# Kernel tuning notes

Measured on AMD Instinct MI355X. Metric: run time of the kernel, lower is better.

## Reference

```python
import jax, jax.numpy as jnp
import numpy as np

NUM_HEADS = 16
D_MODEL = 1024
BATCH = 4
SEQ = 1024


def setup_inputs() -> dict:
    key = jax.random.key(0)
    k_x, k_m, k_wqkv, k_bqkv, k_wo, k_bo = jax.random.split(key, 6)
    d = D_MODEL
    scale = 1.0 / np.sqrt(d)
    return {
        "x": jax.random.normal(k_x, (BATCH, SEQ, d), dtype=jnp.float32),
        "mask": jax.random.randint(k_m, (BATCH, SEQ, SEQ), 0, 2, dtype=jnp.int32),
        "Wqkv": jax.random.normal(k_wqkv, (d, 3 * d), dtype=jnp.float32) * scale,
        "bqkv": jax.random.normal(k_bqkv, (3 * d,), dtype=jnp.float32) * 0.02,
        "Wo": jax.random.normal(k_wo, (d, d), dtype=jnp.float32) * scale,
        "bo": jax.random.normal(k_bo, (d,), dtype=jnp.float32) * 0.02,
    }


def reference(x, mask, Wqkv, bqkv, Wo, bo):
    B, S, D = x.shape
    H = NUM_HEADS
    hd = D // H
    # fused QKV projection: [B,S,3D] -> [B,S,H,3*hd] -> [B,H,S,3*hd]
    qkv = (x @ Wqkv + bqkv).reshape(B, S, H, 3 * hd).transpose(0, 2, 1, 3)
    q, k, v = jnp.split(qkv, 3, axis=-1)  # each [B,H,S,hd]
    # scores [B,H,S,S], scaled by sqrt(head_dim)
    scores = jnp.einsum("bhqd,bhkd->bhqk", q, k) / jnp.sqrt(jnp.float32(hd))
    scores = jnp.where(mask[:, None, :, :] == 0, jnp.float32(-1e20), scores)
    attn = jax.nn.softmax(scores, axis=-1)
    vals = jnp.einsum("bhqk,bhkd->bhqd", attn, v)  # [B,H,S,hd]
    vals = vals.transpose(0, 2, 1, 3).reshape(B, S, D)
    return vals @ Wo + bo
```

## Files before the change

kernel.cpp:

```cpp
#include <hip/hip_runtime.h>
#include <cstddef>
#include <cstdint>

#define BATCH 4
#define SEQ   1024
#define DM    1024
#define NH    16
#define HD    64
#define D3    3072
#define LOG2E 1.44269504088896340736f
#define QSCALE (0.125f * LOG2E)

typedef _Float16 f16x8 __attribute__((ext_vector_type(8)));
typedef _Float16 f16x4 __attribute__((ext_vector_type(4)));
typedef __fp16   h16x2 __attribute__((ext_vector_type(2)));
typedef float    f32x4 __attribute__((ext_vector_type(4)));

#define MFMA16(a, b, c) __builtin_amdgcn_mfma_f32_16x16x32_f16((a), (b), (c), 0, 0, 0)
#define GLD_LDS16(gp, lp) \
  __builtin_amdgcn_global_load_lds((const __attribute__((address_space(1))) unsigned int*)(gp), \
                                   (__attribute__((address_space(3))) unsigned int*)(lp), 16, 0, 0)
#if __has_builtin(__builtin_amdgcn_exp2f)
#define EXP2(x) __builtin_amdgcn_exp2f(x)
#else
#define EXP2(x) exp2f(x)
#endif

__global__ __launch_bounds__(256) void prep(const float* __restrict__ x,
                                            _Float16* __restrict__ x16,
                                            const int* __restrict__ mask,
                                            unsigned long long* __restrict__ mb) {
  const int tid = threadIdx.x;
  if (blockIdx.x < 2048) {
    const int i = blockIdx.x * 256 + tid;
    float4 a = ((const float4*)x)[i * 2];
    float4 b = ((const float4*)x)[i * 2 + 1];
    f16x8 o;
    o[0] = (_Float16)a.x; o[1] = (_Float16)a.y; o[2] = (_Float16)a.z; o[3] = (_Float16)a.w;
    o[4] = (_Float16)b.x; o[5] = (_Float16)b.y; o[6] = (_Float16)b.z; o[7] = (_Float16)b.w;
    ((f16x8*)x16)[i] = o;
  } else {
    const size_t i = (size_t)(blockIdx.x - 2048) * 256 + tid;
    const int m = mask[i];
    unsigned long long bits = __ballot(m != 0);
    if ((tid & 63) == 0) mb[i >> 6] = bits;
  }
}

__global__ __launch_bounds__(256) void transpose_cast2(const float* __restrict__ W1,
                                                       _Float16* __restrict__ WT1,
                                                       const float* __restrict__ W2,
                                                       _Float16* __restrict__ WT2) {
  __shared__ _Float16 T[64 * 72];
  const int tid = threadIdx.x;
  const bool first = blockIdx.x < 48;
  const float* W = first ? W1 : W2;
  _Float16* WT = first ? WT1 : WT2;
  const int N = first ? D3 : DM;
  const int K = DM;
  const int c0 = (first ? blockIdx.x : (blockIdx.x - 48)) * 64;
  const int r0 = blockIdx.y * 64;
#pragma unroll
  for (int it = 0; it < 4; ++it) {
    const int row = it * 16 + (tid >> 4);
    const int col4 = (tid & 15) * 4;
    float4 wv = *(const float4*)(W + (size_t)(r0 + row) * N + c0 + col4);
    T[(col4 + 0) * 72 + row] = (_Float16)wv.x;
    T[(col4 + 1) * 72 + row] = (_Float16)wv.y;
    T[(col4 + 2) * 72 + row] = (_Float16)wv.z;
    T[(col4 + 3) * 72 + row] = (_Float16)wv.w;
  }
  __syncthreads();
#pragma unroll
  for (int it = 0; it < 2; ++it) {
    const int g = it * 256 + tid;
    const int col = g >> 3, seg = g & 7;
    *(f16x8*)(WT + (size_t)(c0 + col) * K + r0 + seg * 8) = *(const f16x8*)(T + col * 72 + seg * 8);
  }
}

template <typename OutT, bool QKV, int TN>
__global__ __launch_bounds__(256) void gemm_bt(const _Float16* __restrict__ A,
                                               const _Float16* __restrict__ BT,
                                               const float* __restrict__ bias,
                                               OutT* __restrict__ C,
                                               _Float16* __restrict__ vTp,
                                               int M, int N, int K) {
  constexpr int NT = TN / 32;
  __shared__ _Float16 As[128 * 64];
  __shared__ _Float16 Bs[TN * 64];
  const int tid = threadIdx.x;
  const int l15 = tid & 15;
  const int quad = (tid & 63) >> 4;
  const int w = tid >> 6;
  const int wm = w >> 1, wn = w & 1;
  const int rowbase = blockIdx.y * 128;
  const int colbase = blockIdx.x * TN;

  f32x4 acc[4][NT];
#pragma unroll
  for (int mt = 0; mt < 4; ++mt)
#pragma unroll
    for (int nt = 0; nt < NT; ++nt) acc[mt][nt] = (f32x4){0.f, 0.f, 0.f, 0.f};

  for (int k0 = 0; k0 < K; k0 += 64) {
    __syncthreads();
#pragma unroll
    for (int it = 0; it < 4; ++it) {
      const int g = it * 256 + tid;
      const int r = g >> 3, cs = (g & 7) ^ (r & 7);
      GLD_LDS16(A + (size_t)(rowbase + r) * K + k0 + cs * 8, As + g * 8);
    }
#pragma unroll
    for (int it = 0; it < TN / 32; ++it) {
      const int g = it * 256 + tid;
      const int r = g >> 3, cs = (g & 7) ^ (r & 7);
      GLD_LDS16(BT + (size_t)(colbase + r) * K + k0 + cs * 8, Bs + g * 8);
    }
    __syncthreads();
#pragma unroll
    for (int kh = 0; kh < 2; ++kh) {
      f16x8 a[4], b[NT];
#pragma unroll
      for (int mt = 0; mt < 4; ++mt) {
        const int row = wm * 64 + mt * 16 + l15;
        a[mt] = *(const f16x8*)(As + row * 64 + (((kh * 4 + quad) ^ (row & 7)) << 3));
      }
#pragma unroll
      for (int nt = 0; nt < NT; ++nt) {
        const int row = wn * (TN / 2) + nt * 16 + l15;
        b[nt] = *(const f16x8*)(Bs + row * 64 + (((kh * 4 + quad) ^ (row & 7)) << 3));
      }
#pragma unroll
      for (int mt = 0; mt < 4; ++mt)
#pragma unroll
        for (int nt = 0; nt < NT; ++nt)
          acc[mt][nt] = MFMA16(a[mt], b[nt], acc[mt][nt]);
    }
  }

  float bv[NT];
#pragma unroll
  for (int nt = 0; nt < NT; ++nt) bv[nt] = bias[colbase + wn * (TN / 2) + nt * 16 + l15];
#pragma unroll
  for (int mt = 0; mt < 4; ++mt)
#pragma unroll
    for (int nt = 0; nt < NT; ++nt) {
      const int col = colbase + wn * (TN / 2) + nt * 16 + l15;
      if (QKV) {
        const int reg3 = (col >> 6) % 3;
        if (reg3 == 2) {
          const int hh = col / 192;
          const int d = col - hh * 192 - 128;
          const int row0 = rowbase + wm * 64 + mt * 16 + quad * 4;
          const int bb = row0 >> 10, s0 = row0 & 1023;
          f16x4 pk;
#pragma unroll
          for (int r = 0; r < 4; ++r) pk[r] = (_Float16)(acc[mt][nt][r] + bv[nt]);
          *(f16x4*)(vTp + ((size_t)((bb * NH + hh) * HD + d)) * SEQ + s0) = pk;
        } else {
          const float sc = (reg3 == 0) ? QSCALE : 1.f;
#pragma unroll
          for (int r = 0; r < 4; ++r) {
            const int row = rowbase + wm * 64 + mt * 16 + quad * 4 + r;
            C[(size_t)row * N + col] = (OutT)((acc[mt][nt][r] + bv[nt]) * sc);
          }
        }
      } else {
#pragma unroll
        for (int r = 0; r < 4; ++r) {
          const int row = rowbase + wm * 64 + mt * 16 + quad * 4 + r;
          C[(size_t)row * N + col] = (OutT)(acc[mt][nt][r] + bv[nt]);
        }
      }
    }
}

__global__ __launch_bounds__(256) void attn(const _Float16* __restrict__ qkv,
                                            const _Float16* __restrict__ vT,
                                            const unsigned long long* __restrict__ mb,
                                            _Float16* __restrict__ vals) {
  __shared__ _Float16 Ks[64 * 72];
  __shared__ _Float16 Vt[64 * 72];
  __shared__ _Float16 Ps[4][32 * 72];
  __shared__ __align__(8) _Float16 LUT[16][4];
  const int tid = threadIdx.x;
  const int l15 = tid & 15, quad = (tid & 63) >> 4, w = tid >> 6;
  const int i = blockIdx.x;
  const int bh = (i >> 6) * 8 + (i & 7);
  const int b = bh >> 4, h = bh & 15;
  const int q0 = ((i >> 3) & 7) << 7;

  if (tid < 16) {
    LUT[tid][0] = (tid & 1) ? (_Float16)1.f : (_Float16)0.f;
    LUT[tid][1] = (tid & 2) ? (_Float16)1.f : (_Float16)0.f;
    LUT[tid][2] = (tid & 4) ? (_Float16)1.f : (_Float16)0.f;
    LUT[tid][3] = (tid & 8) ? (_Float16)1.f : (_Float16)0.f;
  }

  const _Float16* qb = qkv + (size_t)b * SEQ * D3 + h * 192;
  f16x8 qf[2][2];
#pragma unroll
  for (int qn = 0; qn < 2; ++qn)
#pragma unroll
    for (int hf = 0; hf < 2; ++hf)
      qf[qn][hf] = *(const f16x8*)(qb + (size_t)(q0 + w * 32 + qn * 16 + l15) * D3 +
                                   hf * 32 + quad * 8);

  const _Float16* kg = qb + 64;
  const _Float16* vg = vT + (size_t)((b * NH + h) * HD) * SEQ;
  const int sr = tid >> 3, sseg = tid & 7;
  const int vd = tid >> 2, vs = tid & 3;
  const size_t mb0 = (size_t)(b * SEQ + q0 + w * 32 + l15) * 16;
  const size_t mb1 = (size_t)(b * SEQ + q0 + w * 32 + 16 + l15) * 16;

  f16x8 k0r = *(const f16x8*)(kg + (size_t)sr * D3 + sseg * 8);
  f16x8 k1r = *(const f16x8*)(kg + (size_t)(sr + 32) * D3 + sseg * 8);
  f16x8 v0r = *(const f16x8*)(vg + (size_t)vd * SEQ + vs * 8);
  f16x8 v1r = *(const f16x8*)(vg + (size_t)vd * SEQ + 32 + vs * 8);
  unsigned long long mr0 = mb[mb0], mr1 = mb[mb1];

  f32x4 lacc[2];
  f32x4 o_[2][4];
#pragma unroll
  for (int qn = 0; qn < 2; ++qn) {
    lacc[qn] = (f32x4){0.f, 0.f, 0.f, 0.f};
#pragma unroll
    for (int dt = 0; dt < 4; ++dt) o_[qn][dt] = (f32x4){0.f, 0.f, 0.f, 0.f};
  }
  f16x8 ones;
#pragma unroll
  for (int i2 = 0; i2 < 8; ++i2) ones[i2] = (_Float16)1.f;

  for (int kt = 0; kt < 16; ++kt) {
    if (kt) __syncthreads();
    *(f16x8*)(Ks + sr * 72 + sseg * 8) = k0r;
    *(f16x8*)(Ks + (sr + 32) * 72 + sseg * 8) = k1r;
    *(f16x8*)(Vt + vd * 72 + vs * 8) = v0r;
    *(f16x8*)(Vt + vd * 72 + 32 + vs * 8) = v1r;
    __syncthreads();
    const unsigned long long mc[2] = {mr0, mr1};
    if (kt < 15) {
      const int kn = (kt + 1) << 6;
      k0r = *(const f16x8*)(kg + (size_t)(kn + sr) * D3 + sseg * 8);
      k1r = *(const f16x8*)(kg + (size_t)(kn + sr + 32) * D3 + sseg * 8);
      v0r = *(const f16x8*)(vg + (size_t)vd * SEQ + kn + vs * 8);
      v1r = *(const f16x8*)(vg + (size_t)vd * SEQ + kn + 32 + vs * 8);
      mr0 = mb[mb0 + kt + 1];
      mr1 = mb[mb1 + kt + 1];
    }
    f32x4 st[4][2];
#pragma unroll
    for (int mt = 0; mt < 4; ++mt)
#pragma unroll
      for (int qn = 0; qn < 2; ++qn) st[mt][qn] = (f32x4){0.f, 0.f, 0.f, 0.f};
#pragma unroll
    for (int mt = 0; mt < 4; ++mt) {
      f16x8 ka0 = *(const f16x8*)(Ks + (mt * 16 + l15) * 72 + quad * 8);
      f16x8 ka1 = *(const f16x8*)(Ks + (mt * 16 + l15) * 72 + 32 + quad * 8);
#pragma unroll
      for (int qn = 0; qn < 2; ++qn) {
        st[mt][qn] = MFMA16(ka0, qf[qn][0], st[mt][qn]);
        st[mt][qn] = MFMA16(ka1, qf[qn][1], st[mt][qn]);
      }
    }
#pragma unroll
    for (int qn = 0; qn < 2; ++qn)
#pragma unroll
      for (int mt = 0; mt < 4; ++mt) {
        float e0 = EXP2(fminf(st[mt][qn][0], 15.f));
        float e1 = EXP2(fminf(st[mt][qn][1], 15.f));
        float e2 = EXP2(fminf(st[mt][qn][2], 15.f));
        float e3 = EXP2(fminf(st[mt][qn][3], 15.f));
        h16x2 lo = __builtin_amdgcn_cvt_pkrtz(e0, e1);
        h16x2 hi = __builtin_amdgcn_cvt_pkrtz(e2, e3);
        f16x4 pk;
        pk[0] = (_Float16)lo[0]; pk[1] = (_Float16)lo[1];
        pk[2] = (_Float16)hi[0]; pk[3] = (_Float16)hi[1];
        const unsigned nib = (unsigned)(mc[qn] >> (mt * 16 + quad * 4)) & 15u;
        pk *= *(const f16x4*)LUT[nib];
        *(f16x4*)(&Ps[w][(qn * 16 + l15) * 72 + mt * 16 + quad * 4]) = pk;
      }
    f16x8 pa[2][2];
#pragma unroll
    for (int qn = 0; qn < 2; ++qn) {
      pa[qn][0] = *(const f16x8*)(&Ps[w][(qn * 16 + l15) * 72 + quad * 8]);
      pa[qn][1] = *(const f16x8*)(&Ps[w][(qn * 16 + l15) * 72 + 32 + quad * 8]);
      lacc[qn] = MFMA16(pa[qn][0], ones, lacc[qn]);
      lacc[qn] = MFMA16(pa[qn][1], ones, lacc[qn]);
    }
#pragma unroll
    for (int dt = 0; dt < 4; ++dt) {
      f16x8 vb0 = *(const f16x8*)(Vt + (dt * 16 + l15) * 72 + quad * 8);
      f16x8 vb1 = *(const f16x8*)(Vt + (dt * 16 + l15) * 72 + 32 + quad * 8);
#pragma unroll
      for (int qn = 0; qn < 2; ++qn) {
        o_[qn][dt] = MFMA16(pa[qn][0], vb0, o_[qn][dt]);
        o_[qn][dt] = MFMA16(pa[qn][1], vb1, o_[qn][dt]);
      }
    }
  }
#pragma unroll
  for (int qn = 0; qn < 2; ++qn) {
    f32x4 inv;
#pragma unroll
    for (int r = 0; r < 4; ++r) inv[r] = 1.f / lacc[qn][r];
#pragma unroll
    for (int dt = 0; dt < 4; ++dt)
#pragma unroll
      for (int r = 0; r < 4; ++r)
        vals[(size_t)(b * SEQ + q0 + w * 32 + qn * 16 + quad * 4 + r) * DM +
             h * HD + dt * 16 + l15] = (_Float16)(o_[qn][dt][r] * inv[r]);
  }
}

extern "C" void kernel_launch(void* const* d_in, const int* in_sizes, int n_in,
                              void* d_out, int out_size, void* d_ws, size_t ws_size,
                              hipStream_t stream) {
  const float* x    = (const float*)d_in[0];
  const int*   mask = (const int*)  d_in[1];
  const float* Wqkv = (const float*)d_in[2];
  const float* bqkv = (const float*)d_in[3];
  const float* Wo   = (const float*)d_in[4];
  const float* bo   = (const float*)d_in[5];
  float* out = (float*)d_out;

  char* ws = (char*)d_ws;
  _Float16* qkv16  = (_Float16*)ws;                    ws += (size_t)BATCH*SEQ*D3*2;
  _Float16* vT16   = (_Float16*)ws;                    ws += (size_t)BATCH*DM*SEQ*2;
  _Float16* x16    = (_Float16*)ws;                    ws += (size_t)BATCH*SEQ*DM*2;
  _Float16* WqkvT  = (_Float16*)ws;                    ws += (size_t)DM*D3*2;
  _Float16* WoT    = (_Float16*)ws;                    ws += (size_t)DM*DM*2;
  _Float16* vals16 = (_Float16*)ws;                    ws += (size_t)BATCH*SEQ*DM*2;
  unsigned long long* mbits = (unsigned long long*)ws;

  prep<<<2048 + (BATCH*SEQ*SEQ)/256, 256, 0, stream>>>(x, x16, mask, mbits);
  transpose_cast2<<<dim3(64, 16), 256, 0, stream>>>(Wqkv, WqkvT, Wo, WoT);

  gemm_bt<_Float16, true, 128><<<dim3(D3/128, BATCH*SEQ/128), 256, 0, stream>>>(
      x16, WqkvT, bqkv, qkv16, vT16, BATCH*SEQ, D3, DM);
  attn<<<512, 256, 0, stream>>>(qkv16, vT16, mbits, vals16);
  gemm_bt<float, false, 64><<<dim3(DM/64, (BATCH*SEQ)/128), 256, 0, stream>>>(
      vals16, WoT, bo, out, nullptr, BATCH*SEQ, DM, DM);
}
```

Baseline: 185.8 us.

## Merge weight transpose into prep and mask bit-packing into QKV GEMM launch

Folds the weight transpose-cast into the x-cast prep kernel and moves the mask-to-bitmask packing into extra blocks of the QKV GEMM launch, cutting five launches to four and letting the bandwidth-bound mask pass overlap with GEMM compute. It also specializes the GEMM templates into separate QKV and output kernels. In attention, the LDS lookup table used for masking is replaced by per-element selects, and the clamp on exp2 inputs is dropped. Removing the clamp risks fp16 overflow when scores are large. The mask blocks also add LDS footprint, since they are launched from a kernel that declares 32KB of shared memory.

```diff
diff --git a/kernel.cpp b/kernel.cpp
--- a/kernel.cpp
+++ b/kernel.cpp
@@ -28,8 +28,11 @@
 
 __global__ __launch_bounds__(256) void prep(const float* __restrict__ x,
                                             _Float16* __restrict__ x16,
-                                            const int* __restrict__ mask,
-                                            unsigned long long* __restrict__ mb) {
+                                            const float* __restrict__ W1,
+                                            _Float16* __restrict__ WT1,
+                                            const float* __restrict__ W2,
+                                            _Float16* __restrict__ WT2) {
+  __shared__ _Float16 T[64 * 72];
   const int tid = threadIdx.x;
   if (blockIdx.x < 2048) {
     const int i = blockIdx.x * 256 + tid;
@@ -40,68 +43,152 @@
     o[4] = (_Float16)b.x; o[5] = (_Float16)b.y; o[6] = (_Float16)b.z; o[7] = (_Float16)b.w;
     ((f16x8*)x16)[i] = o;
   } else {
-    const size_t i = (size_t)(blockIdx.x - 2048) * 256 + tid;
+    const int idx = blockIdx.x - 2048;
+    const int ct = idx & 63, rt = idx >> 6;
+    const bool first = ct < 48;
+    const float* W = first ? W1 : W2;
+    _Float16* WT = first ? WT1 : WT2;
+    const int N = first ? D3 : DM;
+    const int K = DM;
+    const int c0 = (first ? ct : (ct - 48)) * 64;
+    const int r0 = rt * 64;
+#pragma unroll
+    for (int it = 0; it < 4; ++it) {
+      const int row = it * 16 + (tid >> 4);
+      const int col4 = (tid & 15) * 4;
+      float4 wv = *(const float4*)(W + (size_t)(r0 + row) * N + c0 + col4);
+      T[(col4 + 0) * 72 + row] = (_Float16)wv.x;
+      T[(col4 + 1) * 72 + row] = (_Float16)wv.y;
+      T[(col4 + 2) * 72 + row] = (_Float16)wv.z;
+      T[(col4 + 3) * 72 + row] = (_Float16)wv.w;
+    }
+    __syncthreads();
+#pragma unroll
+    for (int it = 0; it < 2; ++it) {
+      const int g = it * 256 + tid;
+      const int col = g >> 3, seg = g & 7;
+      *(f16x8*)(WT + (size_t)(c0 + col) * K + r0 + seg * 8) =
+          *(const f16x8*)(T + col * 72 + seg * 8);
+    }
+  }
+}
+
+__global__ __launch_bounds__(256) void gemm_qkv(const _Float16* __restrict__ A,
+                                                const _Float16* __restrict__ BT,
+                                                const float* __restrict__ bias,
+                                                _Float16* __restrict__ C,
+                                                _Float16* __restrict__ vTp,
+                                                const int* __restrict__ mask,
+                                                unsigned long long* __restrict__ mb) {
+  __shared__ _Float16 As[128 * 64];
+  __shared__ _Float16 Bs[128 * 64];
+  const int tid = threadIdx.x;
+  if (blockIdx.x >= 768) {
+    const size_t i = (size_t)(blockIdx.x - 768) * 256 + tid;
     const int m = mask[i];
     unsigned long long bits = __ballot(m != 0);
     if ((tid & 63) == 0) mb[i >> 6] = bits;
-  }
+    return;
+  }
+  const int K = DM, N = D3;
+  const int l15 = tid & 15;
+  const int quad = (tid & 63) >> 4;
+  const int w = tid >> 6;
+  const int wm = w >> 1, wn = w & 1;
+  const int rowbase = (blockIdx.x / 24) * 128;
+  const int colbase = (blockIdx.x % 24) * 128;
+
+  f32x4 acc[4][4];
+#pragma unroll
+  for (int mt = 0; mt < 4; ++mt)
+#pragma unroll
+    for (int nt = 0; nt < 4; ++nt) acc[mt][nt] = (f32x4){0.f, 0.f, 0.f, 0.f};
+
+  for (int k0 = 0; k0 < K; k0 += 64) {
+    __syncthreads();
+#pragma unroll
+    for (int it = 0; it < 4; ++it) {
+      const int g = it * 256 + tid;
+      const int r = g >> 3, cs = (g & 7) ^ (r & 7);
+      GLD_LDS16(A + (size_t)(rowbase + r) * K + k0 + cs * 8, As + g * 8);
+    }
+#pragma unroll
+    for (int it = 0; it < 4; ++it) {
+      const int g = it * 256 + tid;
+      const int r = g >> 3, cs = (g & 7) ^ (r & 7);
+      GLD_LDS16(BT + (size_t)(colbase + r) * K + k0 + cs * 8, Bs + g * 8);
+    }
+    __syncthreads();
+#pragma unroll
+    for (int kh = 0; kh < 2; ++kh) {
+      f16x8 a[4], b[4];
+#pragma unroll
+      for (int mt = 0; mt < 4; ++mt) {
+        const int row = wm * 64 + mt * 16 + l15;
+        a[mt] = *(const f16x8*)(As + row * 64 + (((kh * 4 + quad) ^ (row & 7)) << 3));
+      }
+#pragma unroll
+      for (int nt = 0; nt < 4; ++nt) {
+        const int row = wn * 64 + nt * 16 + l15;
+        b[nt] = *(const f16x8*)(Bs + row * 64 + (((kh * 4 + quad) ^ (row & 7)) << 3));
+      }
+#pragma unroll
+      for (int mt = 0; mt < 4; ++mt)
+#pragma unroll
+        for (int nt = 0; nt < 4; ++nt)
+          acc[mt][nt] = MFMA16(a[mt], b[nt], acc[mt][nt]);
+    }
+  }
+
+  float bv[4];
+#pragma unroll
+  for (int nt = 0; nt < 4; ++nt) bv[nt] = bias[colbase + wn * 64 + nt * 16 + l15];
+#pragma unroll
+  for (int mt = 0; mt < 4; ++mt)
+#pragma unroll
+    for (int nt = 0; nt < 4; ++nt) {
+      const int col = colbase + wn * 64 + nt * 16 + l15;
+      const int reg3 = (col >> 6) % 3;
+      if (reg3 == 2) {
+        const int hh = col / 192;
+        const int d = col - hh * 192 - 128;
+        const int row0 = rowbase + wm * 64 + mt * 16 + quad * 4;
+        const int bb = row0 >> 10, s0 = row0 & 1023;
+        f16x4 pk;
+#pragma unroll
+        for (int r = 0; r < 4; ++r) pk[r] = (_Float16)(acc[mt][nt][r] + bv[nt]);
+        *(f16x4*)(vTp + ((size_t)((bb * NH + hh) * HD + d)) * SEQ + s0) = pk;
+      } else {
+        const float sc = (reg3 == 0) ? QSCALE : 1.f;
+#pragma unroll
+        for (int r = 0; r < 4; ++r) {
+          const int row = rowbase + wm * 64 + mt * 16 + quad * 4 + r;
+          C[(size_t)row * N + col] = (_Float16)((acc[mt][nt][r] + bv[nt]) * sc);
+        }
+      }
+    }
 }
 
-__global__ __launch_bounds__(256) void transpose_cast2(const float* __restrict__ W1,
-                                                       _Float16* __restrict__ WT1,
-                                                       const float* __restrict__ W2,
-                                                       _Float16* __restrict__ WT2) {
-  __shared__ _Float16 T[64 * 72];
-  const int tid = threadIdx.x;
-  const bool first = blockIdx.x < 48;
-  const float* W = first ? W1 : W2;
-  _Float16* WT = first ? WT1 : WT2;
-  const int N = first ? D3 : DM;
-  const int K = DM;
-  const int c0 = (first ? blockIdx.x : (blockIdx.x - 48)) * 64;
-  const int r0 = blockIdx.y * 64;
-#pragma unroll
-  for (int it = 0; it < 4; ++it) {
-    const int row = it * 16 + (tid >> 4);
-    const int col4 = (tid & 15) * 4;
-    float4 wv = *(const float4*)(W + (size_t)(r0 + row) * N + c0 + col4);
-    T[(col4 + 0) * 72 + row] = (_Float16)wv.x;
-    T[(col4 + 1) * 72 + row] = (_Float16)wv.y;
-    T[(col4 + 2) * 72 + row] = (_Float16)wv.z;
-    T[(col4 + 3) * 72 + row] = (_Float16)wv.w;
-  }
-  __syncthreads();
-#pragma unroll
-  for (int it = 0; it < 2; ++it) {
-    const int g = it * 256 + tid;
-    const int col = g >> 3, seg = g & 7;
-    *(f16x8*)(WT + (size_t)(c0 + col) * K + r0 + seg * 8) = *(const f16x8*)(T + col * 72 + seg * 8);
-  }
-}
-
-template <typename OutT, bool QKV, int TN>
-__global__ __launch_bounds__(256) void gemm_bt(const _Float16* __restrict__ A,
-                                               const _Float16* __restrict__ BT,
-                                               const float* __restrict__ bias,
-                                               OutT* __restrict__ C,
-                                               _Float16* __restrict__ vTp,
-                                               int M, int N, int K) {
-  constexpr int NT = TN / 32;
+__global__ __launch_bounds__(256) void gemm_out(const _Float16* __restrict__ A,
+                                                const _Float16* __restrict__ BT,
+                                                const float* __restrict__ bias,
+                                                float* __restrict__ C) {
   __shared__ _Float16 As[128 * 64];
-  __shared__ _Float16 Bs[TN * 64];
+  __shared__ _Float16 Bs[64 * 64];
+  const int K = DM, N = DM;
   const int tid = threadIdx.x;
   const int l15 = tid & 15;
   const int quad = (tid & 63) >> 4;
   const int w = tid >> 6;
   const int wm = w >> 1, wn = w & 1;
   const int rowbase = blockIdx.y * 128;
-  const int colbase = blockIdx.x * TN;
-
-  f32x4 acc[4][NT];
+  const int colbase = blockIdx.x * 64;
+
+  f32x4 acc[4][2];
 #pragma unroll
   for (int mt = 0; mt < 4; ++mt)
 #pragma unroll
-    for (int nt = 0; nt < NT; ++nt) acc[mt][nt] = (f32x4){0.f, 0.f, 0.f, 0.f};
+    for (int nt = 0; nt < 2; ++nt) acc[mt][nt] = (f32x4){0.f, 0.f, 0.f, 0.f};
 
   for (int k0 = 0; k0 < K; k0 += 64) {
     __syncthreads();
@@ -111,67 +198,50 @@
       const int r = g >> 3, cs = (g & 7) ^ (r & 7);
       GLD_LDS16(A + (size_t)(rowbase + r) * K + k0 + cs * 8, As + g * 8);
     }
-#pragma unroll
-    for (int it = 0; it < TN / 32; ++it) {
-      const int g = it * 256 + tid;
+    {
+      const int g = tid;
       const int r = g >> 3, cs = (g & 7) ^ (r & 7);
       GLD_LDS16(BT + (size_t)(colbase + r) * K + k0 + cs * 8, Bs + g * 8);
     }
+    {
+      const int g = 256 + tid;
+      const int r = g >> 3, cs = (g & 7) ^ (r & 7);
+      GLD_LDS16(BT + (size_t)(colbase + r) * K + k0 + cs * 8, Bs + g * 8);
+    }
     __syncthreads();
 #pragma unroll
     for (int kh = 0; kh < 2; ++kh) {
-      f16x8 a[4], b[NT];
+      f16x8 a[4], b[2];
 #pragma unroll
       for (int mt = 0; mt < 4; ++mt) {
         const int row = wm * 64 + mt * 16 + l15;
         a[mt] = *(const f16x8*)(As + row * 64 + (((kh * 4 + quad) ^ (row & 7)) << 3));
       }
 #pragma unroll
-      for (int nt = 0; nt < NT; ++nt) {
-        const int row = wn * (TN / 2) + nt * 16 + l15;
+      for (int nt = 0; nt < 2; ++nt) {
+        const int row = wn * 32 + nt * 16 + l15;
         b[nt] = *(const f16x8*)(Bs + row * 64 + (((kh * 4 + quad) ^ (row & 7)) << 3));
       }
 #pragma unroll
       for (int mt = 0; mt < 4; ++mt)
 #pragma unroll
-        for (int nt = 0; nt < NT; ++nt)
+        for (int nt = 0; nt < 2; ++nt)
           acc[mt][nt] = MFMA16(a[mt], b[nt], acc[mt][nt]);
     }
   }
 
-  float bv[NT];
-#pragma unroll
-  for (int nt = 0; nt < NT; ++nt) bv[nt] = bias[colbase + wn * (TN / 2) + nt * 16 + l15];
+  float bv[2];
+#pragma unroll
+  for (int nt = 0; nt < 2; ++nt) bv[nt] = bias[colbase + wn * 32 + nt * 16 + l15];
 #pragma unroll
   for (int mt = 0; mt < 4; ++mt)
 #pragma unroll
-    for (int nt = 0; nt < NT; ++nt) {
-      const int col = colbase + wn * (TN / 2) + nt * 16 + l15;
-      if (QKV) {
-        const int reg3 = (col >> 6) % 3;
-        if (reg3 == 2) {
-          const int hh = col / 192;
-          const int d = col - hh * 192 - 128;
-          const int row0 = rowbase + wm * 64 + mt * 16 + quad * 4;
-          const int bb = row0 >> 10, s0 = row0 & 1023;
-          f16x4 pk;
-#pragma unroll
-          for (int r = 0; r < 4; ++r) pk[r] = (_Float16)(acc[mt][nt][r] + bv[nt]);
-          *(f16x4*)(vTp + ((size_t)((bb * NH + hh) * HD + d)) * SEQ + s0) = pk;
-        } else {
-          const float sc = (reg3 == 0) ? QSCALE : 1.f;
-#pragma unroll
-          for (int r = 0; r < 4; ++r) {
-            const int row = rowbase + wm * 64 + mt * 16 + quad * 4 + r;
-            C[(size_t)row * N + col] = (OutT)((acc[mt][nt][r] + bv[nt]) * sc);
-          }
-        }
-      } else {
-#pragma unroll
-        for (int r = 0; r < 4; ++r) {
-          const int row = rowbase + wm * 64 + mt * 16 + quad * 4 + r;
-          C[(size_t)row * N + col] = (OutT)(acc[mt][nt][r] + bv[nt]);
-        }
+    for (int nt = 0; nt < 2; ++nt) {
+      const int col = colbase + wn * 32 + nt * 16 + l15;
+#pragma unroll
+      for (int r = 0; r < 4; ++r) {
+        const int row = rowbase + wm * 64 + mt * 16 + quad * 4 + r;
+        C[(size_t)row * N + col] = acc[mt][nt][r] + bv[nt];
       }
     }
 }
@@ -183,20 +253,12 @@
   __shared__ _Float16 Ks[64 * 72];
   __shared__ _Float16 Vt[64 * 72];
   __shared__ _Float16 Ps[4][32 * 72];
-  __shared__ __align__(8) _Float16 LUT[16][4];
   const int tid = threadIdx.x;
   const int l15 = tid & 15, quad = (tid & 63) >> 4, w = tid >> 6;
   const int i = blockIdx.x;
   const int bh = (i >> 6) * 8 + (i & 7);
   const int b = bh >> 4, h = bh & 15;
   const int q0 = ((i >> 3) & 7) << 7;
-
-  if (tid < 16) {
-    LUT[tid][0] = (tid & 1) ? (_Float16)1.f : (_Float16)0.f;
-    LUT[tid][1] = (tid & 2) ? (_Float16)1.f : (_Float16)0.f;
-    LUT[tid][2] = (tid & 4) ? (_Float16)1.f : (_Float16)0.f;
-    LUT[tid][3] = (tid & 8) ? (_Float16)1.f : (_Float16)0.f;
-  }
 
   const _Float16* qb = qkv + (size_t)b * SEQ * D3 + h * 192;
   f16x8 qf[2][2];
@@ -268,17 +330,20 @@
     for (int qn = 0; qn < 2; ++qn)
 #pragma unroll
       for (int mt = 0; mt < 4; ++mt) {
-        float e0 = EXP2(fminf(st[mt][qn][0], 15.f));
-        float e1 = EXP2(fminf(st[mt][qn][1], 15.f));
-        float e2 = EXP2(fminf(st[mt][qn][2], 15.f));
-        float e3 = EXP2(fminf(st[mt][qn][3], 15.f));
+        const unsigned nib = (unsigned)(mc[qn] >> (mt * 16 + quad * 4)) & 15u;
+        float e0 = EXP2(st[mt][qn][0]);
+        float e1 = EXP2(st[mt][qn][1]);
+        float e2 = EXP2(st[mt][qn][2]);
+        float e3 = EXP2(st[mt][qn][3]);
+        e0 = (nib & 1u) ? e0 : 0.f;
+        e1 = (nib & 2u) ? e1 : 0.f;
+        e2 = (nib & 4u) ? e2 : 0.f;
+        e3 = (nib & 8u) ? e3 : 0.f;
         h16x2 lo = __builtin_amdgcn_cvt_pkrtz(e0, e1);
         h16x2 hi = __builtin_amdgcn_cvt_pkrtz(e2, e3);
         f16x4 pk;
         pk[0] = (_Float16)lo[0]; pk[1] = (_Float16)lo[1];
         pk[2] = (_Float16)hi[0]; pk[3] = (_Float16)hi[1];
-        const unsigned nib = (unsigned)(mc[qn] >> (mt * 16 + quad * 4)) & 15u;
-        pk *= *(const f16x4*)LUT[nib];
         *(f16x4*)(&Ps[w][(qn * 16 + l15) * 72 + mt * 16 + quad * 4]) = pk;
       }
     f16x8 pa[2][2];
@@ -334,12 +399,9 @@
   _Float16* vals16 = (_Float16*)ws;                    ws += (size_t)BATCH*SEQ*DM*2;
   unsigned long long* mbits = (unsigned long long*)ws;
 
-  prep<<<2048 + (BATCH*SEQ*SEQ)/256, 256, 0, stream>>>(x, x16, mask, mbits);
-  transpose_cast2<<<dim3(64, 16), 256, 0, stream>>>(Wqkv, WqkvT, Wo, WoT);
-
-  gemm_bt<_Float16, true, 128><<<dim3(D3/128, BATCH*SEQ/128), 256, 0, stream>>>(
-      x16, WqkvT, bqkv, qkv16, vT16, BATCH*SEQ, D3, DM);
+  prep<<<2048 + 1024, 256, 0, stream>>>(x, x16, Wqkv, WqkvT, Wo, WoT);
+  gemm_qkv<<<768 + (BATCH*SEQ*SEQ)/256, 256, 0, stream>>>(
+      x16, WqkvT, bqkv, qkv16, vT16, mask, mbits);
   attn<<<512, 256, 0, stream>>>(qkv16, vT16, mbits, vals16);
-  gemm_bt<float, false, 64><<<dim3(DM/64, (BATCH*SEQ)/128), 256, 0, stream>>>(
-      vals16, WoT, bo, out, nullptr, BATCH*SEQ, DM, DM);
+  gemm_out<<<dim3(DM/64, (BATCH*SEQ)/128), 256, 0, stream>>>(vals16, WoT, bo, out);
 }
```

New measurement: 196.4 us. +5.7%, slower.
